# Performance work log

Hardware: AMD Instinct MI355X
Metric: run time of the kernel (lower is better)

## Reference

```python
import jax, jax.numpy as jnp
import numpy as np

D = 384; QK = 48; E = 768; LOCAL = E - D
NB = 8; NTOK = 100; NEG = -1e30
B = 128; S = 100; NPTS = 256


def layernorm(x, w, eps=1e-5):
    mu = jnp.mean(x, axis=-1, keepdims=True)
    var = jnp.mean((x - mu) ** 2, axis=-1, keepdims=True)
    return (x - mu) * jax.lax.rsqrt(var + eps) * w


def attend(q, k, v, bias=None):
    scale = 1.0 / jnp.sqrt(jnp.asarray(q.shape[-1], q.dtype))
    s = jnp.einsum('bqd,bkd->bqk', q, k) * scale
    if bias is not None:
        s = s + bias
    return jnp.einsum('bqk,bkd->bqd', jax.nn.softmax(s, axis=-1), v)


def setup_inputs() -> dict:
    key = jax.random.key(0)
    ks = jax.random.split(key, 16)
    s_exp = 0.5 / (D ** 0.5) / 2.0   # 0.5 / sqrt(residual_depth) / expand_factor
    s_prj = 1.0 / (D ** 0.5) / 2.0 / NB
    return {
        'q': jax.random.randint(ks[0], (B, S), 0, NTOK),
        'pts': jax.random.randint(ks[1], (B, NPTS, 2), 0, NTOK),
        'emb': jax.random.normal(ks[2], (NTOK, D), jnp.float32),
        'pt_emb': jax.random.normal(ks[3], (NTOK, D // 2), jnp.float32),
        'norm_w': jnp.ones((D,), jnp.float32),
        'out_w': jax.random.normal(ks[4], (NTOK, D), jnp.float32) / (D ** 0.5),
        'ln1': jnp.ones((NB, D), jnp.float32),
        'expand': s_exp * jax.random.normal(ks[5], (NB, 2 * QK + 2 * E, D), jnp.float32),
        'project1': s_prj * jax.random.normal(ks[6], (NB, D, E), jnp.float32),
        'bias_mult': jnp.ones((NB,), jnp.float32),
        'ln2': jnp.ones((NB, D), jnp.float32),
        'Wq': s_exp * jax.random.normal(ks[7], (NB, QK + 2 * LOCAL, D), jnp.float32),
        'Wkv': s_exp * jax.random.normal(ks[8], (NB, QK + 2 * D, D), jnp.float32),
        'project2': s_prj * jax.random.normal(ks[9], (NB, D, E), jnp.float32),
    }


def _forward(q, pts, emb, pt_emb, norm_w, out_w, ln1, expand, project1, bias_mult, ln2, Wq, Wkv, project2):
    x = emb[q]                                        # [B,S,D]
    kv = pt_emb[pts].reshape(pts.shape[0], -1, D)     # [B,NPTS,D] (pairs of 2D coords fold into D)
    x = layernorm(x, norm_w)

    pos = jnp.arange(x.shape[1])
    pbb = (pos[None, :] - pos[:, None]).astype(x.dtype)  # position bias base (j - i)
    allowed = pos[None, :] <= pos[:, None]                # causal: attend to past + self

    def step(h, p):
        w_ln1, W_e, W_p1, bm, w_ln2, W_q, W_kv, W_p2 = p
        # --- latent self-attention block ---
        bias = jnp.where(allowed, jax.nn.softplus(bm) * pbb, NEG)
        n = layernorm(h, w_ln1)
        proj = n @ W_e.T                                  # [B,S,2*QK+2*E]
        qr = proj[..., :QK]
        kr = proj[..., QK:2 * QK]
        lin = proj[..., 2 * QK:2 * QK + E]
        pre = proj[..., 2 * QK + E:]
        geglu = lin * jax.nn.gelu(pre, approximate=False)
        attn = attend(qr, kr, geglu[..., LOCAL:], bias)
        h = h + jnp.concatenate([geglu[..., :LOCAL], attn], axis=-1) @ W_p1.T
        # --- latent cross-attention block ---
        n = layernorm(h, w_ln2)
        pq = n @ W_q.T                                    # [B,S,QK+2*LOCAL]
        qr2 = pq[..., :QK]
        g_local = pq[..., QK:QK + LOCAL] * jax.nn.gelu(pq[..., QK + LOCAL:], approximate=False)
        pk = kv @ W_kv.T                                  # [B,NPTS,QK+2*D]
        k2 = pk[..., :QK]
        g_val = pk[..., QK:QK + D] * jax.nn.gelu(pk[..., QK + D:], approximate=False)
        attn2 = attend(qr2, k2, g_val)
        h = h + jnp.concatenate([g_local, attn2], axis=-1) @ W_p2.T
        return h, None

    x, _ = jax.lax.scan(step, x, (ln1, expand, project1, bias_mult, ln2, Wq, Wkv, project2))
    x = layernorm(x, norm_w)
    return x @ out_w.T                                    # [B,S,NTOK]


def reference(q, pts, emb, pt_emb, norm_w, out_w, ln1, expand, project1, bias_mult, ln2, Wq, Wkv, project2):
    return _forward(q, pts, emb, pt_emb, norm_w, out_w, ln1, expand, project1, bias_mult, ln2, Wq, Wkv, project2)
```

## Files before the change

kernel.cpp:

```cpp
#include <hip/hip_runtime.h>
#include <hip/hip_bf16.h>
#include <math.h>

#define B_    128
#define S_    100
#define D_    384
#define QK_   48
#define E_    768
#define LOCAL_ 384
#define NB_   8
#define NTOK_ 100
#define NPTS_ 256
#define M_    (B_*S_)

typedef unsigned short ushort;
typedef __attribute__((ext_vector_type(8))) short  bf16x8;
typedef __attribute__((ext_vector_type(8))) unsigned short ushort8v;
typedef __attribute__((ext_vector_type(4))) float  f32x4;

#define MFMA(a,b,c) __builtin_amdgcn_mfma_f32_16x16x32_bf16(a,b,c,0,0,0)

static __device__ __forceinline__ float gelu_f(float x) {
    float y = 1.5957691216057308f * (x + 0.044715f * x * x * x);
    float e = __expf(y);
    float t = 1.0f - 2.0f / (e + 1.0f);
    return 0.5f * x * (1.0f + t);
}
static __device__ __forceinline__ ushort f2b(float f) {
    union { float f; unsigned u; } x; x.f = f;
    unsigned r = x.u + 0x7FFFu + ((x.u >> 16) & 1u);
    return (ushort)(r >> 16);
}
static __device__ __forceinline__ float b2f(ushort u) {
    union { unsigned u; float f; } x; x.u = ((unsigned)u) << 16;
    return x.f;
}

static __device__ __forceinline__ void xcd_swz(int xn, int gy, int& bx, int& by) {
    int L = blockIdx.x + xn * blockIdx.y;
    int gmain = (gy & ~7) * xn;
    if (L < gmain) {
        int grp = L / (8 * xn);
        int r = L % (8 * xn);
        bx = r >> 3;
        by = grp * 8 + (r & 7);
    } else {
        int Lp = L - gmain;
        int tail = gy & 7;
        by = (gy & ~7) + (Lp % tail);
        bx = Lp / tail;
    }
}

__global__ __launch_bounds__(256)
void ln_rows(const float* __restrict__ X, const float* __restrict__ w,
             ushort* __restrict__ Y, int nrows)
{
    int row = blockIdx.x * 4 + (threadIdx.x >> 6);
    if (row >= nrows) return;
    int lane = threadIdx.x & 63;
    const float* x = X + (size_t)row * D_;
    float v[6]; float s = 0.f;
    #pragma unroll
    for (int t = 0; t < 6; ++t) { v[t] = x[lane + 64*t]; s += v[t]; }
    #pragma unroll
    for (int off = 32; off; off >>= 1) s += __shfl_xor(s, off);
    float mu = s * (1.f/(float)D_);
    float q = 0.f;
    #pragma unroll
    for (int t = 0; t < 6; ++t) { float d = v[t]-mu; q += d*d; }
    #pragma unroll
    for (int off = 32; off; off >>= 1) q += __shfl_xor(q, off);
    float rs = rsqrtf(q * (1.f/(float)D_) + 1e-5f);
    #pragma unroll
    for (int t = 0; t < 6; ++t)
        Y[(size_t)row*D_ + lane + 64*t] = f2b((v[t]-mu)*rs*w[lane + 64*t]);
}

__global__ __launch_bounds__(256)
void x_init(const int* __restrict__ qtok, const float* __restrict__ emb,
            const float* __restrict__ w, float* __restrict__ Y, int nrows)
{
    int row = blockIdx.x * 4 + (threadIdx.x >> 6);
    if (row >= nrows) return;
    int lane = threadIdx.x & 63;
    const float* x = emb + (size_t)qtok[row] * D_;
    float v[6]; float s = 0.f;
    #pragma unroll
    for (int t = 0; t < 6; ++t) { v[t] = x[lane + 64*t]; s += v[t]; }
    #pragma unroll
    for (int off = 32; off; off >>= 1) s += __shfl_xor(s, off);
    float mu = s * (1.f/(float)D_);
    float q = 0.f;
    #pragma unroll
    for (int t = 0; t < 6; ++t) { float d = v[t]-mu; q += d*d; }
    #pragma unroll
    for (int off = 32; off; off >>= 1) q += __shfl_xor(q, off);
    float rs = rsqrtf(q * (1.f/(float)D_) + 1e-5f);
    float* y = Y + (size_t)row * D_;
    #pragma unroll
    for (int t = 0; t < 6; ++t) y[lane + 64*t] = (v[t]-mu)*rs*w[lane + 64*t];
}

#define WE_SZ  (1632*384)
#define P1_SZ  (384*768)
#define WQ_SZ  (816*384)
#define P2_SZ  (384*768)
#define WTOT   (WE_SZ + P1_SZ + WQ_SZ + P2_SZ)

static __device__ __forceinline__ void wsplit(float v, ushort* wh, ushort* wl, size_t o) {
    ushort h = f2b(v);
    wh[o] = h; wl[o] = f2b(v - b2f(h));
}

__global__ __launch_bounds__(256)
void wconv_all_hi(const float* __restrict__ expand, const float* __restrict__ proj1,
                  const float* __restrict__ wq, const float* __restrict__ proj2,
                  ushort* __restrict__ wh)
{
    int i = blockIdx.x*256 + threadIdx.x;
    if (i >= WTOT) return;
    int blk = blockIdx.y;
    float v;
    if (i < WE_SZ) v = expand[(size_t)blk*WE_SZ + i];
    else if (i < WE_SZ+P1_SZ) v = proj1[(size_t)blk*P1_SZ + (i - WE_SZ)];
    else if (i < WE_SZ+P1_SZ+WQ_SZ) v = wq[(size_t)blk*WQ_SZ + (i - WE_SZ - P1_SZ)];
    else v = proj2[(size_t)blk*P2_SZ + (i - WE_SZ - P1_SZ - WQ_SZ)];
    wh[(size_t)blk*WTOT + i] = f2b(v);
}

__global__ __launch_bounds__(256)
void wconv_hi(const float* __restrict__ we, const float* __restrict__ p1,
              const float* __restrict__ wq, const float* __restrict__ p2,
              ushort* __restrict__ wh)
{
    int i = blockIdx.x*256 + threadIdx.x;
    if (i >= WTOT) return;
    float v;
    if (i < WE_SZ) v = we[i];
    else if (i < WE_SZ+P1_SZ) v = p1[i - WE_SZ];
    else if (i < WE_SZ+P1_SZ+WQ_SZ) v = wq[i - WE_SZ - P1_SZ];
    else v = p2[i - WE_SZ - P1_SZ - WQ_SZ];
    wh[i] = f2b(v);
}

__global__ __launch_bounds__(256)
void wconv1(const float* __restrict__ src, int n,
            ushort* __restrict__ wh, ushort* __restrict__ wl)
{
    int i = blockIdx.x*256 + threadIdx.x;
    if (i >= n) return;
    wsplit(src[i], wh, wl, i);
}

__global__ __launch_bounds__(256)
void pconv(const float* __restrict__ src, ushort* __restrict__ dst)
{
    int i = blockIdx.x*256 + threadIdx.x;
    if (i >= 128*192) return;
    int r = i / 192;
    dst[i] = (r < NTOK_) ? f2b(src[i]) : 0;
}

__global__ __launch_bounds__(256)
void mm_bt64(const ushort* __restrict__ A1, int lda1, int K1,
             const ushort* __restrict__ A2, int lda2,
             const ushort* __restrict__ Wgh, const ushort* __restrict__ Wgl,
             float* __restrict__ C, int ldc, int N, int K, int accum)
{
    __shared__ ushort Ah[64][72], Wh[64][72], Wl[64][72];
    int tid = threadIdx.x;
    int row0 = blockIdx.y*64, col0 = blockIdx.x*64;
    int srow = tid >> 3;
    int sseg = (tid & 7) * 8;
    int wid = tid >> 6, lane = tid & 63;
    int wr = wid >> 1, wc = wid & 1;
    int fr = lane & 15, fg = lane >> 4;
    f32x4 acc[2][2] = {};
    for (int k0 = 0; k0 < K; k0 += 64) {
        ushort8v va[2], vc[2], vd[2];
        #pragma unroll
        for (int p = 0; p < 2; ++p) {
            int r = p*32 + srow;
            int arow = row0 + r;
            int wrow = col0 + r;
            int gk = k0 + sseg;
            if (gk < K1) va[p] = *(const ushort8v*)(A1 + (size_t)arow*lda1 + gk);
            else         va[p] = *(const ushort8v*)(A2 + (size_t)arow*lda2 + (gk-K1));
            if (wrow >= N) wrow = N - 1;
            vc[p] = *(const ushort8v*)(Wgh + (size_t)wrow*K + gk);
            vd[p] = *(const ushort8v*)(Wgl + (size_t)wrow*K + gk);
        }
        __syncthreads();
        #pragma unroll
        for (int p = 0; p < 2; ++p) {
            int r = p*32 + srow;
            *(ushort8v*)&Ah[r][sseg] = va[p];
            *(ushort8v*)&Wh[r][sseg] = vc[p];
            *(ushort8v*)&Wl[r][sseg] = vd[p];
        }
        __syncthreads();
        #pragma unroll
        for (int kk = 0; kk < 64; kk += 32) {
            bf16x8 a[2], b_h[2], b_l[2];
            #pragma unroll
            for (int s = 0; s < 2; ++s) {
                a[s]   = *(const bf16x8*)&Ah[wr*32 + s*16 + fr][kk + fg*8];
                b_h[s] = *(const bf16x8*)&Wh[wc*32 + s*16 + fr][kk + fg*8];
                b_l[s] = *(const bf16x8*)&Wl[wc*32 + s*16 + fr][kk + fg*8];
            }
            #pragma unroll
            for (int s = 0; s < 2; ++s)
                #pragma unroll
                for (int u = 0; u < 2; ++u)
                    acc[s][u] = MFMA(a[s], b_h[u], acc[s][u]);
            #pragma unroll
            for (int s = 0; s < 2; ++s)
                #pragma unroll
                for (int u = 0; u < 2; ++u)
                    acc[s][u] = MFMA(a[s], b_l[u], acc[s][u]);
        }
        __syncthreads();
    }
    #pragma unroll
    for (int s = 0; s < 2; ++s) {
        int r = row0 + wr*32 + s*16 + fg*4;
        #pragma unroll
        for (int u = 0; u < 2; ++u) {
            int c = col0 + wc*32 + u*16 + fr;
            if (c < N) {
                #pragma unroll
                for (int j = 0; j < 4; ++j) {
                    size_t o = (size_t)(r+j)*ldc + c;
                    C[o] = accum ? (C[o] + acc[s][u][j]) : acc[s][u][j];
                }
            }
        }
    }
}

__global__ __launch_bounds__(256)
void mm_bt2(const ushort* __restrict__ A1, int lda1, int K1,
            const ushort* __restrict__ A2, int lda2,
            const ushort* __restrict__ Wgh,
            float* __restrict__ C, int ldc, int N, int K, int accum)
{
    __shared__ ushort As[128*32], Whs[64*32];
    int tid = threadIdx.x;
    int lane = tid & 63, wid = tid >> 6;
    int bx, by; xcd_swz(gridDim.x, gridDim.y, bx, by);
    int row0 = by*128, col0 = bx*64;
    int wr = wid >> 1, wc = wid & 1;
    int fr = lane & 15, fg = lane >> 4;
    int gsl = (fg ^ ((fr >> 1) & 3)) * 8;
    int sr = tid >> 2, sg0 = tid & 3;
    int g = sg0 ^ ((sr >> 1) & 3);
    int wrow = col0 + sr; if (wrow >= N) wrow = N - 1;

    ushort8v va[2], vh;
    auto loadk = [&](int k0) {
        const ushort* Asrc; int lda, kk;
        if (k0 < K1) { Asrc = A1; lda = lda1; kk = k0; }
        else         { Asrc = A2; lda = lda2; kk = k0 - K1; }
        #pragma unroll
        for (int i = 0; i < 2; ++i)
            va[i] = *(const ushort8v*)(Asrc + (size_t)(row0 + sr + i*64)*lda + kk + g*8);
        vh = *(const ushort8v*)(Wgh + (size_t)wrow*K + k0 + g*8);
    };

    f32x4 acc[4][2] = {};
    loadk(0);
    for (int k0 = 0; k0 < K; k0 += 32) {
        __syncthreads();
        #pragma unroll
        for (int i = 0; i < 2; ++i)
            *(ushort8v*)&As[(sr + i*64)*32 + sg0*8] = va[i];
        *(ushort8v*)&Whs[sr*32 + sg0*8] = vh;
        if (k0 + 32 < K) loadk(k0 + 32);
        __syncthreads();
        bf16x8 a[4], bh[2];
        #pragma unroll
        for (int s = 0; s < 4; ++s) {
            int r = wr*64 + s*16 + fr;
            a[s] = *(const bf16x8*)&As[r*32 + gsl];
        }
        #pragma unroll
        for (int u = 0; u < 2; ++u) {
            int r = wc*32 + u*16 + fr;
            bh[u] = *(const bf16x8*)&Whs[r*32 + gsl];
        }
        #pragma unroll
        for (int s = 0; s < 4; ++s)
            #pragma unroll
            for (int u = 0; u < 2; ++u)
                acc[s][u] = MFMA(a[s], bh[u], acc[s][u]);
    }
    #pragma unroll
    for (int s = 0; s < 4; ++s) {
        int rb = row0 + wr*64 + s*16 + fg*4;
        #pragma unroll
        for (int u = 0; u < 2; ++u) {
            int c = col0 + wc*32 + u*16 + fr;
            if (c < N) {
                #pragma unroll
                for (int j = 0; j < 4; ++j) {
                    size_t o = (size_t)(rb+j)*ldc + c;
                    C[o] = accum ? (C[o] + acc[s][u][j]) : acc[s][u][j];
                }
            }
        }
    }
}

__global__ __launch_bounds__(256)
void mm_fused2(const ushort* __restrict__ Ag, int lda,
               const ushort* __restrict__ Wqh,
               int Nq, int nqt, float* __restrict__ Qout, int ldq,
               const ushort* __restrict__ W1h, const ushort* __restrict__ W2h,
               ushort* __restrict__ Oh, int ldo, int K)
{
    __shared__ ushort As[128*32];
    __shared__ ushort Xs[2][64*32];
    int tid = threadIdx.x;
    int lane = tid & 63, wid = tid >> 6;
    int bx, by; xcd_swz(gridDim.x, gridDim.y, bx, by);
    int row0 = by*128;
    int wr = wid >> 1, wc = wid & 1;
    int fr = lane & 15, fg = lane >> 4;
    int gsl = (fg ^ ((fr >> 1) & 3)) * 8;
    int sr = tid >> 2, sg0 = tid & 3;
    int g = sg0 ^ ((sr >> 1) & 3);

    if (bx < nqt) {
        int col0 = bx*64;
        int wrow = col0 + sr; if (wrow >= Nq) wrow = Nq - 1;
        ushort8v va[2], vh;
        auto loadk = [&](int k0) {
            #pragma unroll
            for (int i = 0; i < 2; ++i)
                va[i] = *(const ushort8v*)(Ag + (size_t)(row0 + sr + i*64)*lda + k0 + g*8);
            vh = *(const ushort8v*)(Wqh + (size_t)wrow*K + k0 + g*8);
        };
        f32x4 acc[4][2] = {};
        loadk(0);
        for (int k0 = 0; k0 < K; k0 += 32) {
            __syncthreads();
            #pragma unroll
            for (int i = 0; i < 2; ++i)
                *(ushort8v*)&As[(sr + i*64)*32 + sg0*8] = va[i];
            *(ushort8v*)&Xs[0][sr*32 + sg0*8] = vh;
            if (k0 + 32 < K) loadk(k0 + 32);
            __syncthreads();
            bf16x8 a[4], bh[2];
            #pragma unroll
            for (int s = 0; s < 4; ++s) {
                int r = wr*64 + s*16 + fr;
                a[s] = *(const bf16x8*)&As[r*32 + gsl];
            }
            #pragma unroll
            for (int u = 0; u < 2; ++u) {
                int r = wc*32 + u*16 + fr;
                bh[u] = *(const bf16x8*)&Xs[0][r*32 + gsl];
            }
            #pragma unroll
            for (int s = 0; s < 4; ++s)
                #pragma unroll
                for (int u = 0; u < 2; ++u)
                    acc[s][u] = MFMA(a[s], bh[u], acc[s][u]);
        }
        #pragma unroll
        for (int s = 0; s < 4; ++s) {
            int rb = row0 + wr*64 + s*16 + fg*4;
            #pragma unroll
            for (int u = 0; u < 2; ++u) {
                int c = col0 + wc*32 + u*16 + fr;
                if (c < Nq) {
                    #pragma unroll
                    for (int j = 0; j < 4; ++j)
                        Qout[(size_t)(rb+j)*ldq + c] = acc[s][u][j];
                }
            }
        }
    } else {
        int col0 = (bx - nqt)*64;
        ushort8v va[2], vw0, vw2;
        auto loadk = [&](int k0) {
            #pragma unroll
            for (int i = 0; i < 2; ++i)
                va[i] = *(const ushort8v*)(Ag + (size_t)(row0 + sr + i*64)*lda + k0 + g*8);
            size_t wro = (size_t)(col0 + sr)*K + k0 + g*8;
            vw0 = *(const ushort8v*)(W1h + wro);
            vw2 = *(const ushort8v*)(W2h + wro);
        };
        f32x4 acc1[4][2] = {}, acc2[4][2] = {};
        loadk(0);
        for (int k0 = 0; k0 < K; k0 += 32) {
            __syncthreads();
            #pragma unroll
            for (int i = 0; i < 2; ++i)
                *(ushort8v*)&As[(sr + i*64)*32 + sg0*8] = va[i];
            {
                int o = sr*32 + sg0*8;
                *(ushort8v*)&Xs[0][o] = vw0;
                *(ushort8v*)&Xs[1][o] = vw2;
            }
            if (k0 + 32 < K) loadk(k0 + 32);
            __syncthreads();
            bf16x8 a[4], b1[2], b2[2];
            #pragma unroll
            for (int s = 0; s < 4; ++s) {
                int r = wr*64 + s*16 + fr;
                a[s] = *(const bf16x8*)&As[r*32 + gsl];
            }
            #pragma unroll
            for (int u = 0; u < 2; ++u) {
                int r = wc*32 + u*16 + fr;
                b1[u] = *(const bf16x8*)&Xs[0][r*32 + gsl];
                b2[u] = *(const bf16x8*)&Xs[1][r*32 + gsl];
            }
            #pragma unroll
            for (int s = 0; s < 4; ++s)
                #pragma unroll
                for (int u = 0; u < 2; ++u) {
                    acc1[s][u] = MFMA(a[s], b1[u], acc1[s][u]);
                    acc2[s][u] = MFMA(a[s], b2[u], acc2[s][u]);
                }
        }
        #pragma unroll
        for (int s = 0; s < 4; ++s) {
            int rb = row0 + wr*64 + s*16 + fg*4;
            #pragma unroll
            for (int u = 0; u < 2; ++u) {
                int c = col0 + wc*32 + u*16 + fr;
                #pragma unroll
                for (int j = 0; j < 4; ++j) {
                    float gg = acc1[s][u][j] * gelu_f(acc2[s][u][j]);
                    Oh[(size_t)(rb+j)*ldo + c] = f2b(gg);
                }
            }
        }
    }
}

__global__ __launch_bounds__(256)
void pk_mm(const ushort* __restrict__ A,
           const ushort* __restrict__ Wh_, const ushort* __restrict__ Wl_,
           float* __restrict__ P12)
{
    __shared__ ushort Ah[64][72], Wh[64][72], Wl[64][72];
    int tid = threadIdx.x;
    int z = blockIdx.z, blk = z >> 1, half = z & 1;
    int row0 = blockIdx.y*64, col0 = blockIdx.x*64;
    int srow = tid >> 3, sseg = (tid & 7) * 8;
    int wid = tid >> 6, lane = tid & 63;
    int wr = wid >> 1, wc = wid & 1;
    int fr = lane & 15, fg = lane >> 4;
    const ushort* Wbh = Wh_ + (size_t)blk*816*384 + half*192;
    const ushort* Wbl = Wl_ + (size_t)blk*816*384 + half*192;
    float* C = P12 + (size_t)z*128*816;
    f32x4 acc[2][2] = {};
    for (int k0 = 0; k0 < 192; k0 += 64) {
        ushort8v va[2], vc[2], vd[2];
        #pragma unroll
        for (int p = 0; p < 2; ++p) {
            int r = p*32 + srow;
            int wrow = col0 + r; if (wrow >= 816) wrow = 815;
            int gk = k0 + sseg;
            va[p] = *(const ushort8v*)(A + (size_t)(row0 + r)*192 + gk);
            vc[p] = *(const ushort8v*)(Wbh + (size_t)wrow*384 + gk);
            vd[p] = *(const ushort8v*)(Wbl + (size_t)wrow*384 + gk);
        }
        __syncthreads();
        #pragma unroll
        for (int p = 0; p < 2; ++p) {
            int r = p*32 + srow;
            *(ushort8v*)&Ah[r][sseg] = va[p];
            *(ushort8v*)&Wh[r][sseg] = vc[p];
            *(ushort8v*)&Wl[r][sseg] = vd[p];
        }
        __syncthreads();
        #pragma unroll
        for (int kk = 0; kk < 64; kk += 32) {
            bf16x8 a[2], b_h[2], b_l[2];
            #pragma unroll
            for (int s = 0; s < 2; ++s) {
                a[s]   = *(const bf16x8*)&Ah[wr*32 + s*16 + fr][kk + fg*8];
                b_h[s] = *(const bf16x8*)&Wh[wc*32 + s*16 + fr][kk + fg*8];
                b_l[s] = *(const bf16x8*)&Wl[wc*32 + s*16 + fr][kk + fg*8];
            }
            #pragma unroll
            for (int s = 0; s < 2; ++s)
                #pragma unroll
                for (int u = 0; u < 2; ++u)
                    acc[s][u] = MFMA(a[s], b_h[u], acc[s][u]);
            #pragma unroll
            for (int s = 0; s < 2; ++s)
                #pragma unroll
                for (int u = 0; u < 2; ++u)
                    acc[s][u] = MFMA(a[s], b_l[u], acc[s][u]);
        }
        __syncthreads();
    }
    #pragma unroll
    for (int s = 0; s < 2; ++s) {
        int r = row0 + wr*32 + s*16 + fg*4;
        #pragma unroll
        for (int u = 0; u < 2; ++u) {
            int c = col0 + wc*32 + u*16 + fr;
            if (c < 816) {
                #pragma unroll
                for (int j = 0; j < 4; ++j)
                    C[(size_t)(r+j)*816 + c] = acc[s][u][j];
            }
        }
    }
}

__global__ __launch_bounds__(256)
void pv2(const ushort* __restrict__ P, int ldp, long sP,
         const ushort* __restrict__ V, int ldv, long sV,
         ushort* __restrict__ Oh, int ldo, long sO,
         int Mrows, int K, int Kv)
{
    __shared__ ushort Ps[64][40];
    __shared__ ushort Vs[128*32];
    int L = blockIdx.x + gridDim.x*(blockIdx.y + gridDim.y*blockIdx.z);
    int gz = gridDim.z;
    int zz = L % gz;
    int rest = L / gz;
    int bx = rest % gridDim.x;
    int byy = rest / gridDim.x;
    const ushort* Pb = P + (size_t)zz * sP;
    const ushort* Vb = V + (size_t)zz * sV;
    ushort* Ohb = Oh + (size_t)zz * sO;
    int tid = threadIdx.x;
    int row0 = byy*64, col0 = bx*128;
    int wid = tid >> 6, lane = tid & 63;
    int fr = lane & 15, fg = lane >> 4;
    int prow = tid >> 2, pseg = (tid & 3) * 8;
    int vk = tid & 31, vcb = (tid >> 5) * 8;

    ushort8v pv_, vv[2];
    auto loadk = [&](int k0) {
        pv_ = (ushort8v){0,0,0,0,0,0,0,0};
        int grow = row0 + prow;
        if (grow < Mrows)
            pv_ = *(const ushort8v*)(Pb + (size_t)grow*ldp + k0 + pseg);
        vv[0] = (ushort8v){0,0,0,0,0,0,0,0};
        vv[1] = (ushort8v){0,0,0,0,0,0,0,0};
        int gk = k0 + vk;
        if (gk < Kv) {
            #pragma unroll
            for (int i = 0; i < 2; ++i)
                vv[i] = *(const ushort8v*)(Vb + (size_t)gk*ldv + col0 + vcb + i*64);
        }
    };

    f32x4 acc[4][2] = {};
    loadk(0);
    for (int k0 = 0; k0 < K; k0 += 32) {
        __syncthreads();
        *(ushort8v*)&Ps[prow][pseg] = pv_;
        #pragma unroll
        for (int i = 0; i < 2; ++i) {
            #pragma unroll
            for (int e = 0; e < 8; ++e) {
                int c = vcb + i*64 + e;
                Vs[c*32 + (vk & 7) + 8*((vk >> 3) ^ ((c >> 3) & 3))] = vv[i][e];
            }
        }
        if (k0 + 32 < K) loadk(k0 + 32);
        __syncthreads();
        bf16x8 a[4], b[2];
        #pragma unroll
        for (int s = 0; s < 4; ++s)
            a[s] = *(const bf16x8*)&Ps[s*16 + fr][fg*8];
        #pragma unroll
        for (int u = 0; u < 2; ++u) {
            int c = wid*32 + u*16 + fr;
            b[u] = *(const bf16x8*)&Vs[c*32 + 8*(fg ^ ((c >> 3) & 3))];
        }
        #pragma unroll
        for (int s = 0; s < 4; ++s)
            #pragma unroll
            for (int u = 0; u < 2; ++u)
                acc[s][u] = MFMA(a[s], b[u], acc[s][u]);
    }
    #pragma unroll
    for (int s = 0; s < 4; ++s) {
        int rbase = row0 + s*16 + fg*4;
        #pragma unroll
        for (int u = 0; u < 2; ++u) {
            int c = col0 + wid*32 + u*16 + fr;
            #pragma unroll
            for (int j = 0; j < 4; ++j) {
                int r = rbase + j;
                if (r < Mrows)
                    Ohb[(size_t)r*ldo + c] = f2b(acc[s][u][j]);
            }
        }
    }
}

__global__ __launch_bounds__(256)
void attn1_score(const float* __restrict__ qk, const float* __restrict__ bm, int blk,
                 ushort* __restrict__ P)
{
    __shared__ float qrs[50][QK_];
    __shared__ float krs[S_][QK_+1];
    int b = blockIdx.x, r0 = blockIdx.y*50;
    int tid = threadIdx.x;
    for (int idx = tid; idx < 50*QK_; idx += 256) {
        int r = idx / QK_, c = idx % QK_;
        qrs[r][c] = qk[((size_t)(b*S_ + r0 + r))*96 + c];
    }
    for (int idx = tid; idx < S_*QK_; idx += 256) {
        int r = idx / QK_, c = idx % QK_;
        krs[r][c] = qk[((size_t)(b*S_ + r))*96 + 48 + c];
    }
    __syncthreads();
    float bmv = bm[blk];
    float sp = (bmv > 20.f) ? bmv : log1pf(expf(bmv));
    const float scale = 0.14433756729740643f;
    int w = tid >> 6, lane = tid & 63;
    for (int t = 0; t < 13; ++t) {
        int li = w + 4*t;
        if (li >= 50) break;
        int i = r0 + li;
        int j1 = lane, j2 = lane + 64;
        float s1 = -1e30f, s2 = -1e30f;
        if (j1 <= i) {
            float acc = 0.f;
            #pragma unroll
            for (int l = 0; l < QK_; ++l) acc += qrs[li][l]*krs[j1][l];
            s1 = acc*scale + sp*(float)(j1 - i);
        }
        if (j2 <= i) {
            float acc = 0.f;
            #pragma unroll
            for (int l = 0; l < QK_; ++l) acc += qrs[li][l]*krs[j2][l];
            s2 = acc*scale + sp*(float)(j2 - i);
        }
        float m = fmaxf(s1, s2);
        #pragma unroll
        for (int off = 32; off; off >>= 1) m = fmaxf(m, __shfl_xor(m, off));
        float p1 = (j1 <= i) ? expf(s1 - m) : 0.f;
        float p2 = (j2 <= i) ? expf(s2 - m) : 0.f;
        float sum = p1 + p2;
        #pragma unroll
        for (int off = 32; off; off >>= 1) sum += __shfl_xor(sum, off);
        float inv = 1.f / sum;
        ushort* prow = P + ((size_t)(b*S_) + i)*128;
        prow[j1] = f2b(p1*inv);
        prow[j2] = f2b(p2*inv);
    }
}

__global__ __launch_bounds__(256)
void attn2_score(const float* __restrict__ q2, const float* __restrict__ k2,
                 ushort* __restrict__ P)
{
    __shared__ float ks[NPTS_][QK_+1];
    int b = blockIdx.x, r0 = blockIdx.y*20;
    int tid = threadIdx.x;
    for (int idx = tid; idx < NPTS_*QK_; idx += 256) {
        int r = idx / QK_, c = idx % QK_;
        ks[r][c] = k2[((size_t)(b*NPTS_ + r))*QK_ + c];
    }
    __syncthreads();
    const float scale = 0.14433756729740643f;
    int w = tid >> 6, lane = tid & 63;
    for (int t = 0; t < 5; ++t) {
        int i = r0 + w + 4*t;
        const float* qr = q2 + ((size_t)(b*S_ + i))*QK_;
        float s[4] = {0.f,0.f,0.f,0.f};
        for (int l = 0; l < QK_; ++l) {
            float ql = qr[l];
            #pragma unroll
            for (int r = 0; r < 4; ++r) s[r] += ql * ks[lane + 64*r][l];
        }
        #pragma unroll
        for (int r = 0; r < 4; ++r) s[r] *= scale;
        float m = fmaxf(fmaxf(s[0],s[1]), fmaxf(s[2],s[3]));
        #pragma unroll
        for (int off = 32; off; off >>= 1) m = fmaxf(m, __shfl_xor(m, off));
        float p[4]; float sum = 0.f;
        #pragma unroll
        for (int r = 0; r < 4; ++r) { p[r] = expf(s[r]-m); sum += p[r]; }
        #pragma unroll
        for (int off = 32; off; off >>= 1) sum += __shfl_xor(sum, off);
        float inv = 1.f / sum;
        ushort* prow = P + ((size_t)(b*S_) + i)*256;
        #pragma unroll
        for (int r = 0; r < 4; ++r) prow[lane + 64*r] = f2b(p[r]*inv);
    }
}

__global__ __launch_bounds__(256)
void pk_gather(const int* __restrict__ pts, const float* __restrict__ P12, int blk,
               float* __restrict__ k2, ushort* __restrict__ gv)
{
    int pair = blockIdx.x*4 + (threadIdx.x >> 6);
    int lane = threadIdx.x & 63;
    const float* P1 = P12 + (size_t)(blk*2 + 0)*128*816;
    const float* P2 = P12 + (size_t)(blk*2 + 1)*128*816;
    int t0 = pts[2*pair], t1 = pts[2*pair+1];
    const float* a = P1 + (size_t)t0*816;
    const float* c = P2 + (size_t)t1*816;
    if (lane < QK_) k2[(size_t)pair*QK_ + lane] = a[lane] + c[lane];
    #pragma unroll
    for (int t = 0; t < 6; ++t) {
        int i = lane + 64*t;
        float lin = a[48 + i] + c[48 + i];
        float pre = a[432 + i] + c[432 + i];
        gv[(size_t)pair*D_ + i] = f2b(lin * gelu_f(pre));
    }
}

extern "C" void kernel_launch(void* const* d_in, const int* in_sizes, int n_in,
                              void* d_out, int out_size, void* d_ws, size_t ws_size,
                              hipStream_t stream)
{
    const int*   qtok  = (const int*)d_in[0];
    const int*   pts   = (const int*)d_in[1];
    const float* emb   = (const float*)d_in[2];
    const float* ptemb = (const float*)d_in[3];
    const float* normw = (const float*)d_in[4];
    const float* outw  = (const float*)d_in[5];
    const float* ln1   = (const float*)d_in[6];
    const float* expand= (const float*)d_in[7];
    const float* proj1 = (const float*)d_in[8];
    const float* bm    = (const float*)d_in[9];
    const float* ln2   = (const float*)d_in[10];
    const float* Wq    = (const float*)d_in[11];
    const float* Wkv   = (const float*)d_in[12];
    const float* proj2 = (const float*)d_in[13];
    float* out = (float*)d_out;

    char* base = (char*)d_ws;
    size_t off = 0;
    auto alloc = [&](size_t bytes){ void* p = base + off; off += (bytes + 255) & ~(size_t)255; return p; };
    float*  h     = (float*) alloc((size_t)M_*D_*4);
    ushort* nh    = (ushort*)alloc((size_t)M_*D_*2);
    float*  qk1   = (float*) alloc((size_t)M_*96*4);
    ushort* gegl  = (ushort*)alloc((size_t)M_*E_*2);
    ushort* atb   = (ushort*)alloc((size_t)M_*D_*2);
    ushort* Pbuf  = (ushort*)alloc((size_t)M_*256*2);
    ushort* gv    = (ushort*)alloc((size_t)B_*NPTS_*D_*2);
    float*  P12   = (float*) alloc((size_t)16*128*816*4);
    float*  k2    = (float*) alloc((size_t)B_*NPTS_*QK_*4);
    ushort* wkvh  = (ushort*)alloc((size_t)NB_*816*384*2);
    ushort* wkvl  = (ushort*)alloc((size_t)NB_*816*384*2);
    ushort* ptp   = (ushort*)alloc((size_t)128*192*2);
    ushort* obh   = (ushort*)alloc((size_t)NTOK_*D_*2);
    ushort* obl   = (ushort*)alloc((size_t)NTOK_*D_*2);

    size_t rem = (ws_size > off) ? (ws_size - off) : 0;
    bool fits8 = rem >= ((size_t)NB_ * WTOT * 2 + 1024);
    int nlay = fits8 ? NB_ : 1;
    ushort* wbh = (ushort*)alloc((size_t)nlay*WTOT*2);
    size_t wstride = fits8 ? (size_t)WTOT : 0;

    float*  qr2   = qk1;
    ushort* gloc  = gegl;

    const size_t oWE = 0;
    const size_t oP1 = WE_SZ;
    const size_t oWQ = WE_SZ + P1_SZ;
    const size_t oP2 = WE_SZ + P1_SZ + WQ_SZ;

    x_init<<<M_/4, 256, 0, stream>>>(qtok, emb, normw, h, M_);
    pconv<<<(128*192 + 255)/256, 256, 0, stream>>>(ptemb, ptp);
    wconv1<<<(NB_*816*384 + 255)/256, 256, 0, stream>>>(Wkv, NB_*816*384, wkvh, wkvl);
    pk_mm<<<dim3(13, 2, 16), 256, 0, stream>>>(ptp, wkvh, wkvl, P12);
    if (fits8)
        wconv_all_hi<<<dim3((WTOT+255)/256, NB_), 256, 0, stream>>>(
            expand, proj1, Wq, proj2, wbh);

    for (int blk = 0; blk < NB_; ++blk) {
        if (!fits8)
            wconv_hi<<<(WTOT+255)/256, 256, 0, stream>>>(
                expand + (size_t)blk*WE_SZ, proj1 + (size_t)blk*P1_SZ,
                Wq + (size_t)blk*WQ_SZ, proj2 + (size_t)blk*P2_SZ, wbh);
        const ushort* Lh = wbh + wstride*blk;

        ln_rows<<<M_/4, 256, 0, stream>>>(h, ln1 + blk*D_, nh, M_);
        mm_fused2<<<dim3(14, M_/128), 256, 0, stream>>>(nh, D_,
            Lh + oWE, 96, 2, qk1, 96,
            Lh + oWE + (size_t)96*D_, Lh + oWE + (size_t)864*D_,
            gegl, E_, D_);
        attn1_score<<<dim3(B_,2), 256, 0, stream>>>(qk1, bm, blk, Pbuf);
        pv2<<<dim3(3,2,B_), 256, 0, stream>>>(Pbuf, 128, (long)S_*128,
            gegl + LOCAL_, E_, (long)S_*E_,
            atb, D_, (long)S_*D_, S_, 128, S_);
        mm_bt2<<<dim3(6, M_/128), 256, 0, stream>>>(gegl, E_, D_, atb, D_,
            Lh + oP1, h, D_, D_, E_, 1);

        ln_rows<<<M_/4, 256, 0, stream>>>(h, ln2 + blk*D_, nh, M_);
        mm_fused2<<<dim3(7, M_/128), 256, 0, stream>>>(nh, D_,
            Lh + oWQ, 48, 1, qr2, 48,
            Lh + oWQ + (size_t)48*D_, Lh + oWQ + (size_t)432*D_,
            gloc, D_, D_);
        pk_gather<<<B_*NPTS_/4, 256, 0, stream>>>(pts, P12, blk, k2, gv);
        attn2_score<<<dim3(B_,5), 256, 0, stream>>>(qr2, k2, Pbuf);
        pv2<<<dim3(3,2,B_), 256, 0, stream>>>(Pbuf, 256, (long)S_*256,
            gv, D_, (long)NPTS_*D_,
            atb, D_, (long)S_*D_, S_, 256, 256);
        mm_bt2<<<dim3(6, M_/128), 256, 0, stream>>>(gloc, D_, D_, atb, D_,
            Lh + oP2, h, D_, D_, E_, 1);
    }

    ln_rows<<<M_/4, 256, 0, stream>>>(h, normw, nh, M_);
    wconv1<<<(NTOK_*D_ + 255)/256, 256, 0, stream>>>(outw, NTOK_*D_, obh, obl);
    mm_bt64<<<dim3(2, M_/64), 256, 0, stream>>>(nh, D_, D_, nh, D_,
        obh, obl, out, NTOK_, NTOK_, D_, 0);
}
```

Before: 1.658 ms.

## Fuse attention score/softmax into PV kernel using MFMA for QK^T

Replaces the separate scalar-FP32 score+softmax kernels and the P buffer round trip with a single fused kernel. It computes QK^T with bf16 MFMA in shared memory, applies softmax in registers, and stores P to LDS before the PV matmul. This removes two launches per layer and the global write/read of the probability matrix. The cost is that scores are recomputed for each of the 3 column blocks, Q/K are rounded to bf16, and LDS use is larger.

```diff
diff --git a/kernel.cpp b/kernel.cpp
--- a/kernel.cpp
+++ b/kernel.cpp
@@ -516,68 +516,136 @@
     }
 }
 
-__global__ __launch_bounds__(256)
-void pv2(const ushort* __restrict__ P, int ldp, long sP,
-         const ushort* __restrict__ V, int ldv, long sV,
-         ushort* __restrict__ Oh, int ldo, long sO,
-         int Mrows, int K, int Kv)
-{
-    __shared__ ushort Ps[64][40];
+template<int NK, int CAUSAL>
+__global__ __launch_bounds__(256)
+void pv_fused(const float* __restrict__ Q, int ldq,
+              const float* __restrict__ Kf, int ldk, int koff, long sK,
+              const ushort* __restrict__ V, int ldv, long sV,
+              ushort* __restrict__ Oh, int ldo, long sO,
+              int Mrows, int Kv,
+              const float* __restrict__ bm, int blk)
+{
+    constexpr int NKF = NK / 16;
+    constexpr int PSTR = NK + 8;
+    __shared__ ushort SH[64*72 + NK*72];
     __shared__ ushort Vs[128*32];
+    ushort* Qs = SH;
+    ushort* Ks = SH + 64*72;
+    ushort* Pf = SH;
+
     int L = blockIdx.x + gridDim.x*(blockIdx.y + gridDim.y*blockIdx.z);
     int gz = gridDim.z;
     int zz = L % gz;
     int rest = L / gz;
     int bx = rest % gridDim.x;
     int byy = rest / gridDim.x;
-    const ushort* Pb = P + (size_t)zz * sP;
-    const ushort* Vb = V + (size_t)zz * sV;
-    ushort* Ohb = Oh + (size_t)zz * sO;
+    int row0 = byy*64, col0 = bx*128;
+
     int tid = threadIdx.x;
-    int row0 = byy*64, col0 = bx*128;
-    int wid = tid >> 6, lane = tid & 63;
+    int wv = tid >> 6, lane = tid & 63;
     int fr = lane & 15, fg = lane >> 4;
-    int prow = tid >> 2, pseg = (tid & 3) * 8;
-    int vk = tid & 31, vcb = (tid >> 5) * 8;
-
-    ushort8v pv_, vv[2];
-    auto loadk = [&](int k0) {
-        pv_ = (ushort8v){0,0,0,0,0,0,0,0};
-        int grow = row0 + prow;
-        if (grow < Mrows)
-            pv_ = *(const ushort8v*)(Pb + (size_t)grow*ldp + k0 + pseg);
+
+    const float scale = 0.14433756729740643f;
+    float sp = 0.f;
+    if (CAUSAL) { float bmv = bm[blk]; sp = (bmv > 20.f) ? bmv : log1pf(expf(bmv)); }
+
+    const float* Qb = Q + ((size_t)zz * S_) * ldq;
+    for (int idx = tid; idx < 64*64; idx += 256) {
+        int r = idx >> 6, c = idx & 63;
+        int grow = row0 + r; if (grow >= S_) grow = S_ - 1;
+        ushort v = 0;
+        if (c < 48) v = f2b(Qb[(size_t)grow*ldq + c]);
+        Qs[r*72 + c] = v;
+    }
+    const float* Kb = Kf + (size_t)zz*sK + koff;
+    for (int idx = tid; idx < NK*64; idx += 256) {
+        int j = idx >> 6, c = idx & 63;
+        ushort v = 0;
+        if (c < 48 && j < Kv) v = f2b(Kb[(size_t)j*ldk + c]);
+        Ks[j*72 + c] = v;
+    }
+    int vk = tid & 31, vcb = (tid >> 5)*8;
+    ushort8v vv[2];
+    auto loadV = [&](int k0) {
         vv[0] = (ushort8v){0,0,0,0,0,0,0,0};
         vv[1] = (ushort8v){0,0,0,0,0,0,0,0};
         int gk = k0 + vk;
         if (gk < Kv) {
-            #pragma unroll
-            for (int i = 0; i < 2; ++i)
-                vv[i] = *(const ushort8v*)(Vb + (size_t)gk*ldv + col0 + vcb + i*64);
+            const ushort* Vb = V + (size_t)zz*sV;
+            #pragma unroll
+            for (int i2 = 0; i2 < 2; ++i2)
+                vv[i2] = *(const ushort8v*)(Vb + (size_t)gk*ldv + col0 + vcb + i2*64);
         }
     };
+    loadV(0);
+    __syncthreads();
+
+    f32x4 sacc[NKF];
+    #pragma unroll
+    for (int kf = 0; kf < NKF; ++kf) sacc[kf] = (f32x4){0.f,0.f,0.f,0.f};
+    bf16x8 aq0 = *(const bf16x8*)&Qs[(wv*16 + fr)*72 +  0 + fg*8];
+    bf16x8 aq1 = *(const bf16x8*)&Qs[(wv*16 + fr)*72 + 32 + fg*8];
+    #pragma unroll
+    for (int kf = 0; kf < NKF; ++kf) {
+        bf16x8 bk0 = *(const bf16x8*)&Ks[(kf*16 + fr)*72 +  0 + fg*8];
+        bf16x8 bk1 = *(const bf16x8*)&Ks[(kf*16 + fr)*72 + 32 + fg*8];
+        sacc[kf] = MFMA(aq0, bk0, sacc[kf]);
+        sacc[kf] = MFMA(aq1, bk1, sacc[kf]);
+    }
+    #pragma unroll
+    for (int j = 0; j < 4; ++j) {
+        int i = row0 + wv*16 + fg*4 + j;
+        float m = -1e30f;
+        #pragma unroll
+        for (int kf = 0; kf < NKF; ++kf) {
+            int key = kf*16 + fr;
+            float s = sacc[kf][j] * scale;
+            if (CAUSAL) s = (key <= i) ? (s + sp*(float)(key - i)) : -1e30f;
+            sacc[kf][j] = s;
+            m = fmaxf(m, s);
+        }
+        #pragma unroll
+        for (int off = 1; off < 16; off <<= 1) m = fmaxf(m, __shfl_xor(m, off));
+        float sum = 0.f;
+        #pragma unroll
+        for (int kf = 0; kf < NKF; ++kf) {
+            float p = __expf(sacc[kf][j] - m);
+            sacc[kf][j] = p;
+            sum += p;
+        }
+        #pragma unroll
+        for (int off = 1; off < 16; off <<= 1) sum += __shfl_xor(sum, off);
+        float inv = 1.f / sum;
+        #pragma unroll
+        for (int kf = 0; kf < NKF; ++kf) sacc[kf][j] *= inv;
+    }
+    __syncthreads();
+    #pragma unroll
+    for (int j = 0; j < 4; ++j)
+        #pragma unroll
+        for (int kf = 0; kf < NKF; ++kf)
+            Pf[(wv*16 + fg*4 + j)*PSTR + kf*16 + fr] = f2b(sacc[kf][j]);
+    __syncthreads();
 
     f32x4 acc[4][2] = {};
-    loadk(0);
-    for (int k0 = 0; k0 < K; k0 += 32) {
-        __syncthreads();
-        *(ushort8v*)&Ps[prow][pseg] = pv_;
-        #pragma unroll
-        for (int i = 0; i < 2; ++i) {
+    for (int k0 = 0; k0 < NK; k0 += 32) {
+        #pragma unroll
+        for (int i2 = 0; i2 < 2; ++i2) {
             #pragma unroll
             for (int e = 0; e < 8; ++e) {
-                int c = vcb + i*64 + e;
-                Vs[c*32 + (vk & 7) + 8*((vk >> 3) ^ ((c >> 3) & 3))] = vv[i][e];
-            }
-        }
-        if (k0 + 32 < K) loadk(k0 + 32);
+                int c = vcb + i2*64 + e;
+                Vs[c*32 + (vk & 7) + 8*((vk >> 3) ^ ((c >> 3) & 3))] = vv[i2][e];
+            }
+        }
+        if (k0 + 32 < NK) loadV(k0 + 32);
         __syncthreads();
         bf16x8 a[4], b[2];
         #pragma unroll
         for (int s = 0; s < 4; ++s)
-            a[s] = *(const bf16x8*)&Ps[s*16 + fr][fg*8];
+            a[s] = *(const bf16x8*)&Pf[(s*16 + fr)*PSTR + k0 + fg*8];
         #pragma unroll
         for (int u = 0; u < 2; ++u) {
-            int c = wid*32 + u*16 + fr;
+            int c = wv*32 + u*16 + fr;
             b[u] = *(const bf16x8*)&Vs[c*32 + 8*(fg ^ ((c >> 3) & 3))];
         }
         #pragma unroll
@@ -585,13 +653,15 @@
             #pragma unroll
             for (int u = 0; u < 2; ++u)
                 acc[s][u] = MFMA(a[s], b[u], acc[s][u]);
-    }
+        __syncthreads();
+    }
+    ushort* Ohb = Oh + (size_t)zz*sO;
     #pragma unroll
     for (int s = 0; s < 4; ++s) {
         int rbase = row0 + s*16 + fg*4;
         #pragma unroll
         for (int u = 0; u < 2; ++u) {
-            int c = col0 + wid*32 + u*16 + fr;
+            int c = col0 + wv*32 + u*16 + fr;
             #pragma unroll
             for (int j = 0; j < 4; ++j) {
                 int r = rbase + j;
@@ -599,100 +669,6 @@
                     Ohb[(size_t)r*ldo + c] = f2b(acc[s][u][j]);
             }
         }
-    }
-}
-
-__global__ __launch_bounds__(256)
-void attn1_score(const float* __restrict__ qk, const float* __restrict__ bm, int blk,
-                 ushort* __restrict__ P)
-{
-    __shared__ float qrs[50][QK_];
-    __shared__ float krs[S_][QK_+1];
-    int b = blockIdx.x, r0 = blockIdx.y*50;
-    int tid = threadIdx.x;
-    for (int idx = tid; idx < 50*QK_; idx += 256) {
-        int r = idx / QK_, c = idx % QK_;
-        qrs[r][c] = qk[((size_t)(b*S_ + r0 + r))*96 + c];
-    }
-    for (int idx = tid; idx < S_*QK_; idx += 256) {
-        int r = idx / QK_, c = idx % QK_;
-        krs[r][c] = qk[((size_t)(b*S_ + r))*96 + 48 + c];
-    }
-    __syncthreads();
-    float bmv = bm[blk];
-    float sp = (bmv > 20.f) ? bmv : log1pf(expf(bmv));
-    const float scale = 0.14433756729740643f;
-    int w = tid >> 6, lane = tid & 63;
-    for (int t = 0; t < 13; ++t) {
-        int li = w + 4*t;
-        if (li >= 50) break;
-        int i = r0 + li;
-        int j1 = lane, j2 = lane + 64;
-        float s1 = -1e30f, s2 = -1e30f;
-        if (j1 <= i) {
-            float acc = 0.f;
-            #pragma unroll
-            for (int l = 0; l < QK_; ++l) acc += qrs[li][l]*krs[j1][l];
-            s1 = acc*scale + sp*(float)(j1 - i);
-        }
-        if (j2 <= i) {
-            float acc = 0.f;
-            #pragma unroll
-            for (int l = 0; l < QK_; ++l) acc += qrs[li][l]*krs[j2][l];
-            s2 = acc*scale + sp*(float)(j2 - i);
-        }
-        float m = fmaxf(s1, s2);
-        #pragma unroll
-        for (int off = 32; off; off >>= 1) m = fmaxf(m, __shfl_xor(m, off));
-        float p1 = (j1 <= i) ? expf(s1 - m) : 0.f;
-        float p2 = (j2 <= i) ? expf(s2 - m) : 0.f;
-        float sum = p1 + p2;
-        #pragma unroll
-        for (int off = 32; off; off >>= 1) sum += __shfl_xor(sum, off);
-        float inv = 1.f / sum;
-        ushort* prow = P + ((size_t)(b*S_) + i)*128;
-        prow[j1] = f2b(p1*inv);
-        prow[j2] = f2b(p2*inv);
-    }
-}
-
-__global__ __launch_bounds__(256)
-void attn2_score(const float* __restrict__ q2, const float* __restrict__ k2,
-                 ushort* __restrict__ P)
-{
-    __shared__ float ks[NPTS_][QK_+1];
-    int b = blockIdx.x, r0 = blockIdx.y*20;
-    int tid = threadIdx.x;
-    for (int idx = tid; idx < NPTS_*QK_; idx += 256) {
-        int r = idx / QK_, c = idx % QK_;
-        ks[r][c] = k2[((size_t)(b*NPTS_ + r))*QK_ + c];
-    }
-    __syncthreads();
-    const float scale = 0.14433756729740643f;
-    int w = tid >> 6, lane = tid & 63;
-    for (int t = 0; t < 5; ++t) {
-        int i = r0 + w + 4*t;
-        const float* qr = q2 + ((size_t)(b*S_ + i))*QK_;
-        float s[4] = {0.f,0.f,0.f,0.f};
-        for (int l = 0; l < QK_; ++l) {
-            float ql = qr[l];
-            #pragma unroll
-            for (int r = 0; r < 4; ++r) s[r] += ql * ks[lane + 64*r][l];
-        }
-        #pragma unroll
-        for (int r = 0; r < 4; ++r) s[r] *= scale;
-        float m = fmaxf(fmaxf(s[0],s[1]), fmaxf(s[2],s[3]));
-        #pragma unroll
-        for (int off = 32; off; off >>= 1) m = fmaxf(m, __shfl_xor(m, off));
-        float p[4]; float sum = 0.f;
-        #pragma unroll
-        for (int r = 0; r < 4; ++r) { p[r] = expf(s[r]-m); sum += p[r]; }
-        #pragma unroll
-        for (int off = 32; off; off >>= 1) sum += __shfl_xor(sum, off);
-        float inv = 1.f / sum;
-        ushort* prow = P + ((size_t)(b*S_) + i)*256;
-        #pragma unroll
-        for (int r = 0; r < 4; ++r) prow[lane + 64*r] = f2b(p[r]*inv);
     }
 }
 
@@ -745,7 +721,6 @@
     float*  qk1   = (float*) alloc((size_t)M_*96*4);
     ushort* gegl  = (ushort*)alloc((size_t)M_*E_*2);
     ushort* atb   = (ushort*)alloc((size_t)M_*D_*2);
-    ushort* Pbuf  = (ushort*)alloc((size_t)M_*256*2);
     ushort* gv    = (ushort*)alloc((size_t)B_*NPTS_*D_*2);
     float*  P12   = (float*) alloc((size_t)16*128*816*4);
     float*  k2    = (float*) alloc((size_t)B_*NPTS_*QK_*4);
@@ -789,10 +764,12 @@
             Lh + oWE, 96, 2, qk1, 96,
             Lh + oWE + (size_t)96*D_, Lh + oWE + (size_t)864*D_,
             gegl, E_, D_);
-        attn1_score<<<dim3(B_,2), 256, 0, stream>>>(qk1, bm, blk, Pbuf);
-        pv2<<<dim3(3,2,B_), 256, 0, stream>>>(Pbuf, 128, (long)S_*128,
+        pv_fused<128,1><<<dim3(3,2,B_), 256, 0, stream>>>(
+            qk1, 96,
+            qk1, 96, 48, (long)S_*96,
             gegl + LOCAL_, E_, (long)S_*E_,
-            atb, D_, (long)S_*D_, S_, 128, S_);
+            atb, D_, (long)S_*D_,
+            S_, S_, bm, blk);
         mm_bt2<<<dim3(6, M_/128), 256, 0, stream>>>(gegl, E_, D_, atb, D_,
             Lh + oP1, h, D_, D_, E_, 1);
 
@@ -802,10 +779,12 @@
             Lh + oWQ + (size_t)48*D_, Lh + oWQ + (size_t)432*D_,
             gloc, D_, D_);
         pk_gather<<<B_*NPTS_/4, 256, 0, stream>>>(pts, P12, blk, k2, gv);
-        attn2_score<<<dim3(B_,5), 256, 0, stream>>>(qr2, k2, Pbuf);
-        pv2<<<dim3(3,2,B_), 256, 0, stream>>>(Pbuf, 256, (long)S_*256,
+        pv_fused<256,0><<<dim3(3,2,B_), 256, 0, stream>>>(
+            qr2, 48,
+            k2, 48, 0, (long)NPTS_*48,
             gv, D_, (long)NPTS_*D_,
-            atb, D_, (long)S_*D_, S_, 256, 256);
+            atb, D_, (long)S_*D_,
+            S_, NPTS_, bm, blk);
         mm_bt2<<<dim3(6, M_/128), 256, 0, stream>>>(gloc, D_, D_, atb, D_,
             Lh + oP2, h, D_, D_, E_, 1);
     }
```

Measured after the change: 1.839 ms. 10.9% more time.
